# Performance work log

Measured on AMD Instinct MI355X. Metric: run time of the kernel, lower is better.

Reference implementation:

```python
import jax, jax.numpy as jnp
import numpy as np

B, N, C, K, T = 64, 1024, 256, 512, 64
D_THRESH = 0.5
POWER_ITERS = 20


def _pdist(x):
    # x: [..., K, 3] -> pairwise euclidean distances [..., K, K]
    n = jnp.sum(x * x, axis=-1)
    sq = n[..., :, None] + n[..., None, :] - 2.0 * jnp.einsum('...kc,...lc->...kl', x, x)
    return jnp.sqrt(jnp.maximum(sq, 0.0) + 1e-12)


def _forward(rt, rt_centroids, rt_cls_attn, shift_and_scale, W_in, b_in, W1, b1, W2, b2,
             num_rt, anc_idx, pos_idx, neg_idx):
    valid = jnp.arange(N)[None, :] < num_rt[:, None]                      # [B,N]
    # Normalize.batch_unnormalize: pts * scale + shift on valid tokens
    shift = shift_and_scale[:, None, :3]
    scale = shift_and_scale[:, None, 3:4]
    cent = jnp.where(valid[..., None], rt_centroids * scale + shift, rt_centroids)
    attn = jnp.where(valid, rt_cls_attn, -1e9)
    _, top_idx = jax.lax.top_k(attn, K)                                   # [B,K]
    cent_k = jnp.take_along_axis(cent, top_idx[..., None], axis=1)        # [B,K,3]
    rt_k = jnp.take_along_axis(rt, top_idx[..., None], axis=1)            # [B,K,C]
    # SGV padding mask [T,2,K,K]: rows masked by anchor count, cols by pos/neg counts
    n_eff = jnp.minimum(num_rt, K)
    r = jnp.arange(K)
    row_mask = r[None, :] < n_eff[anc_idx][:, None]                       # [T,K]
    col_mask = jnp.stack([r[None, :] < n_eff[pos_idx][:, None],
                          r[None, :] < n_eff[neg_idx][:, None]], axis=1)  # [T,2,K]
    mask = row_mask[:, None, :, None] & col_mask[:, :, None, :]           # [T,2,K,K]
    # input_linear on anchor / neighbour relay tokens
    anc_f = rt_k[anc_idx] @ W_in + b_in                                   # [T,K,C]
    nn_f = jnp.stack([rt_k[pos_idx], rt_k[neg_idx]], axis=1) @ W_in + b_in  # [T,2,K,C]
    anc_c = cent_k[anc_idx]                                               # [T,K,3]
    nn_c = jnp.stack([cent_k[pos_idx], cent_k[neg_idx]], axis=1)          # [T,2,K,3]
    # feature-space nearest-neighbour correspondences anc -> nn (SpectralGV style)
    fd = (jnp.sum(anc_f ** 2, -1)[:, None, :, None]
          + jnp.sum(nn_f ** 2, -1)[:, :, None, :]
          - 2.0 * jnp.einsum('tkc,tnlc->tnkl', anc_f, nn_f))              # [T,2,K,K]
    corr = jnp.argmin(fd, axis=-1)                                        # [T,2,K]
    q_c = jnp.take_along_axis(nn_c, corr[..., None], axis=2)              # [T,2,K,3]
    q_f = jnp.take_along_axis(nn_f, corr[..., None], axis=2)              # [T,2,K,C]
    # correspondence confidence from feature cosine similarity
    cos = jnp.sum(anc_f[:, None] * q_f, -1) / (
        jnp.linalg.norm(anc_f, axis=-1)[:, None] * jnp.linalg.norm(q_f, axis=-1) + 1e-8)
    s = jax.nn.relu(cos)                                                  # [T,2,K]
    # threshold-masked geometric consistency adjacency
    d_p = _pdist(anc_c)[:, None]                                          # [T,1,K,K]
    d_q = _pdist(q_c)                                                     # [T,2,K,K]
    geo = (jnp.abs(d_p - d_q) < D_THRESH) & mask & (~jnp.eye(K, dtype=bool))
    A = geo.astype(jnp.float32) * s[..., :, None] * s[..., None, :]       # [T,2,K,K]
    # leading eigenvector via power iteration (A is entrywise nonnegative)
    v = jnp.full((T, 2, K), 1.0 / np.sqrt(K), dtype=jnp.float32)
    for _ in range(POWER_ITERS):
        w = jnp.einsum('tnkl,tnl->tnk', A, v)
        v = w / (jnp.linalg.norm(w, axis=-1, keepdims=True) + 1e-8)
    eig = -jnp.sort(-v, axis=-1)                                          # sort_eigvec, descending
    h = jax.nn.relu(eig @ W1 + b1)
    scores = jax.nn.sigmoid(h @ W2 + b2)                                  # [T,2,1]
    targets = jnp.zeros_like(scores).at[:, 0].set(1.0)
    return scores, targets


def setup_inputs() -> dict:
    key = jax.random.key(0)
    ks = jax.random.split(key, 12)
    return {
        'rt': jax.random.normal(ks[0], (B, N, C), jnp.float32),
        'rt_centroids': jax.random.normal(ks[1], (B, N, 3), jnp.float32),
        'rt_cls_attn': jax.random.uniform(ks[2], (B, N), jnp.float32),
        'shift_and_scale': jax.random.uniform(ks[3], (B, 4), jnp.float32),
        'num_rt': jax.random.randint(ks[4], (B,), 128, N, jnp.int32),
        'anc_idx': jax.random.randint(ks[5], (T,), 0, B, jnp.int32),
        'pos_idx': jax.random.randint(ks[6], (T,), 0, B, jnp.int32),
        'neg_idx': jax.random.randint(ks[7], (T,), 0, B, jnp.int32),
        'W_in': jax.random.normal(ks[8], (C, C), jnp.float32) / np.sqrt(C),
        'b_in': jnp.zeros((C,), jnp.float32),
        'W1': jax.random.normal(ks[9], (K, K), jnp.float32) / np.sqrt(K),
        'b1': jnp.zeros((K,), jnp.float32),
        'W2': jax.random.normal(ks[10], (K, 1), jnp.float32) / np.sqrt(K),
        'b2': jnp.zeros((1,), jnp.float32),
    }


def reference(rt, rt_centroids, rt_cls_attn, shift_and_scale, num_rt, anc_idx, pos_idx, neg_idx,
              W_in, b_in, W1, b1, W2, b2):
    return _forward(rt, rt_centroids, rt_cls_attn, shift_and_scale, W_in, b_in, W1, b1, W2, b2,
                    num_rt, anc_idx, pos_idx, neg_idx)
```

## Files before the change

### kernel.cpp

```cpp
#include <hip/hip_runtime.h>
#include <cstddef>

#define BB 64
#define NN 1024
#define CC 256
#define KK 512
#define TT 64
#define NPAIR 128

typedef _Float16 h8 __attribute__((ext_vector_type(8)));
typedef _Float16 h4 __attribute__((ext_vector_type(4)));
typedef float f4 __attribute__((ext_vector_type(4)));

typedef __attribute__((address_space(1))) const void GV;
typedef __attribute__((address_space(3))) void LV;
#define GLDS16(g, s) __builtin_amdgcn_global_load_lds((GV*)(const void*)(g), (LV*)(void*)(s), 16, 0, 0)


__global__ __launch_bounds__(256) void wtrans_kernel(
    const float* __restrict__ Win, _Float16* __restrict__ wth, _Float16* __restrict__ wtl)
{
    __shared__ float t[64][65];
    const int k0 = blockIdx.x * 64, n0 = blockIdx.y * 64;
    const int tid = threadIdx.x;
    const int c = tid & 63, r0 = tid >> 6;
    for (int r = r0; r < 64; r += 4)
        t[r][c] = Win[(size_t)(k0 + r) * CC + n0 + c];
    __syncthreads();
    for (int r = r0; r < 64; r += 4) {
        float x = t[c][r];
        _Float16 h = (_Float16)x;
        size_t o = (size_t)(n0 + r) * CC + k0 + c;
        wth[o] = h;
        wtl[o] = (_Float16)(x - (float)h);
    }
}

__global__ __launch_bounds__(512) void sel_kernel(
    const float* __restrict__ attn, const float* __restrict__ cents,
    const float* __restrict__ sas, const int* __restrict__ num_rt,
    int* __restrict__ topidx, int* __restrict__ neff, float* __restrict__ centk)
{
    __shared__ unsigned long long keys[1024];
    const int b = blockIdx.x, tid = threadIdx.x;
    const int nr = num_rt[b];
    for (int i = tid; i < 1024; i += 512) {
        float a = (i < nr) ? attn[b * NN + i] : -1e9f;
        unsigned u = __float_as_uint(a);
        u = (u & 0x80000000u) ? ~u : (u | 0x80000000u);
        keys[i] = ((unsigned long long)u << 32) | (unsigned)(0xFFFFFFFFu - (unsigned)i);
    }
    __syncthreads();
    for (int k = 2; k <= 1024; k <<= 1) {
        for (int j = k >> 1; j > 0; j >>= 1) {
            int i = ((tid & ~(j - 1)) << 1) | (tid & (j - 1));
            int p = i | j;
            unsigned long long a = keys[i], c = keys[p];
            bool up = (i & k) == 0;
            if (up ? (a < c) : (a > c)) { keys[i] = c; keys[p] = a; }
            __syncthreads();
        }
    }
    {
        unsigned long long key = keys[tid];
        int idx = (int)(~(unsigned)key);
        float x = cents[(b * NN + idx) * 3 + 0];
        float y = cents[(b * NN + idx) * 3 + 1];
        float z = cents[(b * NN + idx) * 3 + 2];
        if (idx < nr) {
            float sc = sas[b * 4 + 3];
            x = x * sc + sas[b * 4 + 0];
            y = y * sc + sas[b * 4 + 1];
            z = z * sc + sas[b * 4 + 2];
        }
        float nc = x * x + y * y + z * z;
        ((float4*)centk)[b * KK + tid] = make_float4(x, y, z, nc);
        topidx[b * KK + tid] = idx;
    }
    if (tid == 0) neff[b] = (nr < KK) ? nr : KK;
}

__global__ __launch_bounds__(256) void feat_mfma(
    const float* __restrict__ rt, const int* __restrict__ topidx,
    const _Float16* __restrict__ wth, const _Float16* __restrict__ wtl,
    const float* __restrict__ bin,
    _Float16* __restrict__ feath, _Float16* __restrict__ featl)
{
    const int mtile = blockIdx.x, nt = blockIdx.y;
    __shared__ _Float16 Ah[128][32], Al[128][32], Bh[128][32], Bl[128][32];
    __shared__ int tix[128];
    const int tid = threadIdx.x;
    const int w = tid >> 6, lane = tid & 63;
    const int quad = lane >> 4, l16 = lane & 15;
    const int wm = (w >> 1) * 64, wl = (w & 1) * 64;
    const int b = mtile >> 2;
    if (tid < 128) tix[tid] = topidx[mtile * 128 + tid];
    __syncthreads();
    const int arow_i = tid >> 1;
    const int aseg = (tid & 1) * 16;
    const float* arow = rt + ((size_t)b * NN + tix[arow_i]) * CC + aseg;
    _Float16* bsh = (w < 2) ? &Bh[0][0] : &Bl[0][0];
    const _Float16* bplane = (w < 2) ? wth : wtl;
    const int rowi = lane >> 2, chunk = lane & 3;

    f4 acc[4][4];
    #pragma unroll
    for (int i = 0; i < 4; i++)
        #pragma unroll
        for (int j = 0; j < 4; j++)
            acc[i][j] = (f4){0.f, 0.f, 0.f, 0.f};

    for (int k0 = 0; k0 < CC; k0 += 32) {
        __syncthreads();
        #pragma unroll
        for (int jj = 0; jj < 4; jj++) {
            int j = (w & 1) * 4 + jj;
            int row = j * 16 + rowi;
            GLDS16(bplane + (size_t)(nt * 128 + row) * CC + k0 + chunk * 8, bsh + j * 512);
        }
        {
            const float4* src = (const float4*)(arow + k0);
            #pragma unroll
            for (int c = 0; c < 2; c++) {
                float4 p = src[2 * c], q2 = src[2 * c + 1];
                float xv[8] = {p.x, p.y, p.z, p.w, q2.x, q2.y, q2.z, q2.w};
                h8 hv, lv;
                #pragma unroll
                for (int j = 0; j < 8; j++) {
                    _Float16 h = (_Float16)xv[j];
                    hv[j] = h;
                    lv[j] = (_Float16)(xv[j] - (float)h);
                }
                *(h8*)&Ah[arow_i][aseg + c * 8] = hv;
                *(h8*)&Al[arow_i][aseg + c * 8] = lv;
            }
        }
        __syncthreads();
        h8 afh[4], afl[4], bfh[4], bfl[4];
        #pragma unroll
        for (int i = 0; i < 4; i++) {
            int ra = wm + i * 16 + l16;
            int rb = wl + i * 16 + l16;
            afh[i] = *(const h8*)&Ah[ra][quad * 8];
            afl[i] = *(const h8*)&Al[ra][quad * 8];
            bfh[i] = *(const h8*)&Bh[rb][quad * 8];
            bfl[i] = *(const h8*)&Bl[rb][quad * 8];
        }
        #pragma unroll
        for (int i = 0; i < 4; i++)
            #pragma unroll
            for (int j = 0; j < 4; j++) {
                acc[i][j] = __builtin_amdgcn_mfma_f32_16x16x32_f16(afh[i], bfh[j], acc[i][j], 0, 0, 0);
                acc[i][j] = __builtin_amdgcn_mfma_f32_16x16x32_f16(afh[i], bfl[j], acc[i][j], 0, 0, 0);
                acc[i][j] = __builtin_amdgcn_mfma_f32_16x16x32_f16(afl[i], bfh[j], acc[i][j], 0, 0, 0);
            }
    }
    #pragma unroll
    for (int j = 0; j < 4; j++) {
        int col = wl + j * 16 + l16;
        float bj = bin[nt * 128 + col];
        #pragma unroll
        for (int i = 0; i < 4; i++)
            #pragma unroll
            for (int r = 0; r < 4; r++) {
                int row = wm + i * 16 + quad * 4 + r;
                float v = acc[i][j][r] + bj;
                _Float16 h = (_Float16)v;
                size_t o = (size_t)(mtile * 128 + row) * CC + nt * 128 + col;
                feath[o] = h;
                featl[o] = (_Float16)(v - (float)h);
            }
    }
}

__global__ __launch_bounds__(256) void norm_kernel(
    const _Float16* __restrict__ feath, const _Float16* __restrict__ featl,
    float* __restrict__ normF)
{
    int r = blockIdx.x * 4 + (threadIdx.x >> 6);
    int lane = threadIdx.x & 63;
    h4 hv = ((const h4*)(feath + (size_t)r * CC))[lane];
    h4 lv = ((const h4*)(featl + (size_t)r * CC))[lane];
    float s = 0.f;
    #pragma unroll
    for (int j = 0; j < 4; j++) {
        float x = (float)hv[j] + (float)lv[j];
        s += x * x;
    }
    for (int off = 32; off; off >>= 1) s += __shfl_down(s, off);
    if (lane == 0) normF[r] = s;
}

__global__ __launch_bounds__(256) void argmin_mfma(
    const _Float16* __restrict__ feath, const _Float16* __restrict__ featl,
    const float* __restrict__ normF,
    const int* __restrict__ anc, const int* __restrict__ pos, const int* __restrict__ neg,
    float* __restrict__ partv, int* __restrict__ partl, float* __restrict__ partd)
{
    const int lt = blockIdx.x, kt = blockIdx.y, pr = blockIdx.z;
    const int t = pr >> 1, nn2 = pr & 1;
    const int a = anc[t];
    const int bb = nn2 ? neg[t] : pos[t];
    const size_t Abase = ((size_t)a * KK + kt * 128) * CC;
    const size_t Bbase = ((size_t)bb * KK + lt * 128) * CC;
    __shared__ _Float16 Ah[128][32], Al[128][32], Bh[128][32], Bl[128][32];
    __shared__ float rdv[128][2];
    __shared__ int   rdl[128][2];
    __shared__ float rdd[128][2];
    const int tid = threadIdx.x;
    const int w = tid >> 6, lane = tid & 63;
    const int quad = lane >> 4, l16 = lane & 15;
    const int wm = (w >> 1) * 64, wl = (w & 1) * 64;
    const int rowi = lane >> 2, chunk = lane & 3;
    const _Float16* gplane = (w == 0) ? feath + Abase : (w == 1) ? featl + Abase
                           : (w == 2) ? feath + Bbase : featl + Bbase;
    _Float16* splane = (w == 0) ? &Ah[0][0] : (w == 1) ? &Al[0][0]
                     : (w == 2) ? &Bh[0][0] : &Bl[0][0];
    const _Float16* grow = gplane + (size_t)rowi * CC + chunk * 8;

    f4 acc[4][4];
    #pragma unroll
    for (int i = 0; i < 4; i++)
        #pragma unroll
        for (int j = 0; j < 4; j++)
            acc[i][j] = (f4){0.f, 0.f, 0.f, 0.f};

    for (int k0 = 0; k0 < CC; k0 += 32) {
        __syncthreads();
        #pragma unroll
        for (int j = 0; j < 8; j++)
            GLDS16(grow + (size_t)(j * 16) * CC + k0, splane + j * 512);
        __syncthreads();
        h8 afh[4], afl[4], bfh[4], bfl[4];
        #pragma unroll
        for (int i = 0; i < 4; i++) {
            int ra = wm + i * 16 + l16;
            int rb = wl + i * 16 + l16;
            afh[i] = *(const h8*)&Ah[ra][quad * 8];
            afl[i] = *(const h8*)&Al[ra][quad * 8];
            bfh[i] = *(const h8*)&Bh[rb][quad * 8];
            bfl[i] = *(const h8*)&Bl[rb][quad * 8];
        }
        #pragma unroll
        for (int i = 0; i < 4; i++)
            #pragma unroll
            for (int j = 0; j < 4; j++) {
                acc[i][j] = __builtin_amdgcn_mfma_f32_16x16x32_f16(afh[i], bfh[j], acc[i][j], 0, 0, 0);
                acc[i][j] = __builtin_amdgcn_mfma_f32_16x16x32_f16(afh[i], bfl[j], acc[i][j], 0, 0, 0);
                acc[i][j] = __builtin_amdgcn_mfma_f32_16x16x32_f16(afl[i], bfh[j], acc[i][j], 0, 0, 0);
            }
    }
    float nbj[4];
    #pragma unroll
    for (int j = 0; j < 4; j++)
        nbj[j] = normF[(size_t)bb * KK + lt * 128 + wl + j * 16 + l16];
    #pragma unroll
    for (int i = 0; i < 4; i++) {
        #pragma unroll
        for (int r = 0; r < 4; r++) {
            float bv = INFINITY; int bl = 0; float bd = 0.f;
            #pragma unroll
            for (int j = 0; j < 4; j++) {
                float d = acc[i][j][r];
                float v = nbj[j] - 2.f * d;
                int l = lt * 128 + wl + j * 16 + l16;
                if (v < bv) { bv = v; bl = l; bd = d; }
            }
            #pragma unroll
            for (int off = 1; off < 16; off <<= 1) {
                float ov = __shfl_xor(bv, off);
                int   ol = __shfl_xor(bl, off);
                float od = __shfl_xor(bd, off);
                if (ov < bv || (ov == bv && ol < bl)) { bv = ov; bl = ol; bd = od; }
            }
            if (l16 == 0) {
                int row = wm + i * 16 + quad * 4 + r;
                rdv[row][w & 1] = bv;
                rdl[row][w & 1] = bl;
                rdd[row][w & 1] = bd;
            }
        }
    }
    __syncthreads();
    if (tid < 128) {
        float bv = rdv[tid][0]; int bl = rdl[tid][0]; float bd = rdd[tid][0];
        float v1 = rdv[tid][1]; int l1 = rdl[tid][1];
        if (v1 < bv || (v1 == bv && l1 < bl)) { bv = v1; bl = l1; bd = rdd[tid][1]; }
        size_t idx = (((size_t)pr * 4 + kt) * 128 + tid) * 4 + lt;
        partv[idx] = bv; partl[idx] = bl; partd[idx] = bd;
    }
}

__global__ __launch_bounds__(256) void geo_kernel(
    const float* __restrict__ centk,
    const float* __restrict__ partv, const int* __restrict__ partl,
    const float* __restrict__ partd, const float* __restrict__ normF,
    const int* __restrict__ neff,
    const int* __restrict__ anc, const int* __restrict__ pos, const int* __restrict__ neg,
    float* __restrict__ sbuf, unsigned* __restrict__ gmask)
{
    const int kt = blockIdx.x;
    const int lt4 = blockIdx.y;
    const int pair = blockIdx.z;
    const int t = pair >> 1, nn2 = pair & 1;
    const int a = anc[t];
    const int bb2 = (nn2 == 0) ? pos[t] : neg[t];
    const int nea = neff[a], neb = neff[bb2];
    const bool writer = (kt == 0) && (lt4 == 0);
    __shared__ int ci[512];
    __shared__ __align__(16) float4 ca[512], cq[512];
    for (int i = threadIdx.x; i < KK; i += 256) {
        size_t base = ((size_t)pair * KK + i) * 4;
        float bv = partv[base]; int bl = partl[base]; float bd = partd[base];
        #pragma unroll
        for (int lt = 1; lt < 4; lt++) {
            float v = partv[base + lt]; int l = partl[base + lt];
            if (v < bv || (v == bv && l < bl)) { bv = v; bl = l; bd = partd[base + lt]; }
        }
        ci[i] = bl;
        if (writer) {
            float na = normF[(size_t)a * KK + i];
            float nb = normF[(size_t)bb2 * KK + bl];
            float cosv = bd / (sqrtf(na) * sqrtf(nb) + 1e-8f);
            sbuf[pair * KK + i] = fmaxf(cosv, 0.f);
        }
    }
    __syncthreads();
    for (int i = threadIdx.x; i < KK; i += 256) {
        ca[i] = ((const float4*)centk)[a * KK + i];
        cq[i] = ((const float4*)centk)[bb2 * KK + ci[i]];
    }
    __syncthreads();
    const int k = kt * 256 + threadIdx.x;
    float4 pk = ca[k], qk = cq[k];
    bool rowm = k < nea;
    unsigned* outp = gmask + ((size_t)pair * KK + k) * 16 + lt4 * 4;
    for (int w = 0; w < 4; w++) {
        unsigned word = 0;
        #pragma unroll
        for (int bi = 0; bi < 32; bi++) {
            int l = lt4 * 128 + w * 32 + bi;
            float4 pl = ca[l], ql = cq[l];
            float dp2 = pk.w + pl.w - 2.f * (pk.x * pl.x + pk.y * pl.y + pk.z * pl.z);
            float dp = sqrtf(fmaxf(dp2, 0.f) + 1e-12f);
            float dq2 = qk.w + ql.w - 2.f * (qk.x * ql.x + qk.y * ql.y + qk.z * ql.z);
            float dq = sqrtf(fmaxf(dq2, 0.f) + 1e-12f);
            bool g = (fabsf(dp - dq) < 0.5f) && rowm && (l < neb) && (l != k);
            word |= (g ? (1u << bi) : 0u);
        }
        outp[w] = word;
    }
}

__global__ __launch_bounds__(1024, 4) void power_kernel(
    const unsigned* __restrict__ gmask, const float* __restrict__ sbuf,
    const float* __restrict__ W1, const float* __restrict__ b1,
    const float* __restrict__ W2, const float* __restrict__ b2,
    float* __restrict__ out)
{
    const int pair = blockIdx.x;
    const int tid = threadIdx.x;
    const int row = tid & 511;
    const int half = tid >> 9;
    __shared__ __align__(16) float u[512];
    __shared__ float T[64][257];
    __shared__ float pacc[1024];
    __shared__ float red[16];
    __shared__ float ev[512];
    __shared__ float hpart[1024];
    unsigned m[8];
    const unsigned* g = gmask + ((size_t)pair * KK + row) * 16 + half * 8;
    #pragma unroll
    for (int w = 0; w < 8; w++) m[w] = g[w];
    const float s = sbuf[pair * KK + row];
    const int bp = tid & 63;
    const int vh = tid >> 6;
    const int GV_[16] = {0,1,3,2,6,7,5,4,12,13,15,14,10,11,9,8};
    const int GB[15] = {0,1,0,2,0,1,0,3,0,1,0,2,0,1,0};
    const float GS[15] = {1.f,1.f,-1.f,1.f,1.f,-1.f,-1.f,1.f,1.f,1.f,-1.f,-1.f,1.f,-1.f,-1.f};
    float v = 0.044194173824159216f;
    if (half == 0) u[row] = s * v;
    __syncthreads();
    for (int it = 0; it < 20; it++) {
        {
            float4 ulo = *(const float4*)&u[bp * 8];
            float4 uhi = *(const float4*)&u[bp * 8 + 4];
            float ul[4] = {ulo.x, ulo.y, ulo.z, ulo.w};
            float H = 0.f;
            H += (float)((vh >> 0) & 1) * uhi.x;
            H += (float)((vh >> 1) & 1) * uhi.y;
            H += (float)((vh >> 2) & 1) * uhi.z;
            H += (float)((vh >> 3) & 1) * uhi.w;
            float L = 0.f;
            T[bp][vh * 16 + 0] = H;
            #pragma unroll
            for (int k = 1; k < 16; k++) {
                L += GS[k - 1] * ul[GB[k - 1]];
                T[bp][vh * 16 + GV_[k]] = H + L;
            }
        }
        __syncthreads();
        float a0 = 0.f, a1 = 0.f, a2 = 0.f, a3 = 0.f;
        #pragma unroll
        for (int w = 0; w < 8; w++) {
            unsigned mw = m[w];
            const int p0 = half * 32 + w * 4;
            a0 += T[p0 + 0][mw & 255u];
            a1 += T[p0 + 1][(mw >> 8) & 255u];
            a2 += T[p0 + 2][(mw >> 16) & 255u];
            a3 += T[p0 + 3][mw >> 24];
        }
        pacc[tid] = (a0 + a1) + (a2 + a3);
        __syncthreads();
        float wk = s * (pacc[row] + pacc[row + 512]);
        float t2 = wk * wk;
        for (int off = 32; off; off >>= 1) t2 += __shfl_down(t2, off);
        if ((tid & 63) == 0) red[tid >> 6] = t2;
        __syncthreads();
        float tot = 0.f;
        #pragma unroll
        for (int x = 0; x < 16; x++) tot += red[x];
        tot *= 0.5f;
        v = wk / (sqrtf(tot) + 1e-8f);
        if (half == 0) u[row] = s * v;
        __syncthreads();
    }
    if (half == 0) ev[row] = v;
    __syncthreads();
    for (int kk = 2; kk <= 512; kk <<= 1) {
        for (int j = kk >> 1; j; j >>= 1) {
            if (tid < 256) {
                int i = ((tid & ~(j - 1)) << 1) | (tid & (j - 1));
                int p = i | j;
                float x = ev[i], y = ev[p];
                bool up = (i & kk) == 0;
                if (up ? (x < y) : (x > y)) { ev[i] = y; ev[p] = x; }
            }
            __syncthreads();
        }
    }
    const int cbase = half * 256;
    float h = (half == 0) ? b1[row] : 0.f;
    #pragma unroll 8
    for (int l = 0; l < 256; l++)
        h += ev[cbase + l] * W1[(size_t)(cbase + l) * KK + row];
    hpart[tid] = h;
    __syncthreads();
    float term = 0.f;
    if (half == 0) {
        float hv = fmaxf(hpart[row] + hpart[row + 512], 0.f);
        term = hv * W2[row];
    }
    for (int off = 32; off; off >>= 1) term += __shfl_down(term, off);
    if ((tid & 63) == 0) red[tid >> 6] = term;
    __syncthreads();
    if (tid == 0) {
        float sc = 0.f;
        #pragma unroll
        for (int x = 0; x < 16; x++) sc += red[x];
        sc += b2[0];
        out[pair] = 1.f / (1.f + expf(-sc));
        out[NPAIR + pair] = (pair & 1) ? 0.f : 1.f;
    }
}

extern "C" void kernel_launch(void* const* d_in, const int* in_sizes, int n_in,
                              void* d_out, int out_size, void* d_ws, size_t ws_size,
                              hipStream_t stream) {
    (void)in_sizes; (void)n_in; (void)out_size; (void)ws_size;
    const float* rt    = (const float*)d_in[0];
    const float* cents = (const float*)d_in[1];
    const float* attn  = (const float*)d_in[2];
    const float* sas   = (const float*)d_in[3];
    const int* num_rt  = (const int*)d_in[4];
    const int* anc     = (const int*)d_in[5];
    const int* pos     = (const int*)d_in[6];
    const int* neg     = (const int*)d_in[7];
    const float* Win   = (const float*)d_in[8];
    const float* bin   = (const float*)d_in[9];
    const float* W1    = (const float*)d_in[10];
    const float* b1    = (const float*)d_in[11];
    const float* W2    = (const float*)d_in[12];
    const float* b2    = (const float*)d_in[13];

    float* ws = (float*)d_ws;
    _Float16* feath = (_Float16*)ws;
    _Float16* featl = (_Float16*)(ws + 4194304);
    float* normF = ws + 8388608;
    float* centk = ws + 8421376;
    float* sbuf  = ws + 8552448;
    int* topidx  = (int*)(ws + 8617984);
    int* neffp   = (int*)(ws + 8650752);
    unsigned* gmask = (unsigned*)(ws + 8716352);
    _Float16* wth = (_Float16*)(ws + 8716352 + 786432);
    _Float16* wtl = (_Float16*)(ws + 8716352 + 819200);
    float* partv = (float*)(ws + 9764928);
    int*   partl = (int*)(ws + 10027072);
    float* partd = (float*)(ws + 10289216);
    float* out = (float*)d_out;

    wtrans_kernel<<<dim3(4, 4), 256, 0, stream>>>(Win, wth, wtl);
    sel_kernel<<<64, 512, 0, stream>>>(attn, cents, sas, num_rt, topidx, neffp, centk);
    feat_mfma<<<dim3(256, 2), 256, 0, stream>>>(rt, topidx, wth, wtl, bin, feath, featl);
    norm_kernel<<<8192, 256, 0, stream>>>(feath, featl, normF);
    argmin_mfma<<<dim3(4, 4, 128), 256, 0, stream>>>(feath, featl, normF, anc, pos, neg, partv, partl, partd);
    geo_kernel<<<dim3(2, 4, 128), 256, 0, stream>>>(centk, partv, partl, partd, normF, neffp, anc, pos, neg, sbuf, gmask);
    power_kernel<<<128, 1024, 0, stream>>>(gmask, sbuf, W1, b1, W2, b2, out);
}
```

Measured before the change: 378.1 us.

## Double-buffer LDS tiles in argmin MFMA kernel to overlap loads with compute

Replaces the single-buffered shared-memory tiles in the feature-distance argmin kernel with a two-stage ping-pong buffer. The next K-slice is fetched with global_load_lds while MFMAs run on the current slice, and one barrier per iteration replaces two. The reduction scratch arrays now alias the first tile buffer. Shared memory per block doubles to 64KB, which may lower occupancy.

```diff
diff --git a/kernel.cpp b/kernel.cpp
--- a/kernel.cpp
+++ b/kernel.cpp
@@ -203,10 +203,10 @@
     const int bb = nn2 ? neg[t] : pos[t];
     const size_t Abase = ((size_t)a * KK + kt * 128) * CC;
     const size_t Bbase = ((size_t)bb * KK + lt * 128) * CC;
-    __shared__ _Float16 Ah[128][32], Al[128][32], Bh[128][32], Bl[128][32];
-    __shared__ float rdv[128][2];
-    __shared__ int   rdl[128][2];
-    __shared__ float rdd[128][2];
+    __shared__ _Float16 S[2][4][4096];
+    float* rdv = (float*)&S[0][0][0];
+    int*   rdl = (int*)(rdv + 256);
+    float* rdd = (float*)(rdl + 256);
     const int tid = threadIdx.x;
     const int w = tid >> 6, lane = tid & 63;
     const int quad = lane >> 4, l16 = lane & 15;
@@ -214,8 +214,6 @@
     const int rowi = lane >> 2, chunk = lane & 3;
     const _Float16* gplane = (w == 0) ? feath + Abase : (w == 1) ? featl + Abase
                            : (w == 2) ? feath + Bbase : featl + Bbase;
-    _Float16* splane = (w == 0) ? &Ah[0][0] : (w == 1) ? &Al[0][0]
-                     : (w == 2) ? &Bh[0][0] : &Bl[0][0];
     const _Float16* grow = gplane + (size_t)rowi * CC + chunk * 8;
 
     f4 acc[4][4];
@@ -225,21 +223,32 @@
         for (int j = 0; j < 4; j++)
             acc[i][j] = (f4){0.f, 0.f, 0.f, 0.f};
 
+    #pragma unroll
+    for (int j = 0; j < 8; j++)
+        GLDS16(grow + (size_t)(j * 16) * CC, &S[0][w][j * 512]);
+    __syncthreads();
+
+    int cur = 0;
     for (int k0 = 0; k0 < CC; k0 += 32) {
-        __syncthreads();
-        #pragma unroll
-        for (int j = 0; j < 8; j++)
-            GLDS16(grow + (size_t)(j * 16) * CC + k0, splane + j * 512);
-        __syncthreads();
+        const int k1 = k0 + 32;
+        if (k1 < CC) {
+            #pragma unroll
+            for (int j = 0; j < 8; j++)
+                GLDS16(grow + (size_t)(j * 16) * CC + k1, &S[cur ^ 1][w][j * 512]);
+        }
+        const _Float16* Ahc = &S[cur][0][0];
+        const _Float16* Alc = &S[cur][1][0];
+        const _Float16* Bhc = &S[cur][2][0];
+        const _Float16* Blc = &S[cur][3][0];
         h8 afh[4], afl[4], bfh[4], bfl[4];
         #pragma unroll
         for (int i = 0; i < 4; i++) {
             int ra = wm + i * 16 + l16;
             int rb = wl + i * 16 + l16;
-            afh[i] = *(const h8*)&Ah[ra][quad * 8];
-            afl[i] = *(const h8*)&Al[ra][quad * 8];
-            bfh[i] = *(const h8*)&Bh[rb][quad * 8];
-            bfl[i] = *(const h8*)&Bl[rb][quad * 8];
+            afh[i] = *(const h8*)&Ahc[ra * 32 + quad * 8];
+            afl[i] = *(const h8*)&Alc[ra * 32 + quad * 8];
+            bfh[i] = *(const h8*)&Bhc[rb * 32 + quad * 8];
+            bfl[i] = *(const h8*)&Blc[rb * 32 + quad * 8];
         }
         #pragma unroll
         for (int i = 0; i < 4; i++)
@@ -249,6 +258,8 @@
                 acc[i][j] = __builtin_amdgcn_mfma_f32_16x16x32_f16(afh[i], bfl[j], acc[i][j], 0, 0, 0);
                 acc[i][j] = __builtin_amdgcn_mfma_f32_16x16x32_f16(afl[i], bfh[j], acc[i][j], 0, 0, 0);
             }
+        __syncthreads();
+        cur ^= 1;
     }
     float nbj[4];
     #pragma unroll
@@ -275,17 +286,17 @@
             }
             if (l16 == 0) {
                 int row = wm + i * 16 + quad * 4 + r;
-                rdv[row][w & 1] = bv;
-                rdl[row][w & 1] = bl;
-                rdd[row][w & 1] = bd;
+                rdv[row * 2 + (w & 1)] = bv;
+                rdl[row * 2 + (w & 1)] = bl;
+                rdd[row * 2 + (w & 1)] = bd;
             }
         }
     }
     __syncthreads();
     if (tid < 128) {
-        float bv = rdv[tid][0]; int bl = rdl[tid][0]; float bd = rdd[tid][0];
-        float v1 = rdv[tid][1]; int l1 = rdl[tid][1];
-        if (v1 < bv || (v1 == bv && l1 < bl)) { bv = v1; bl = l1; bd = rdd[tid][1]; }
+        float bv = rdv[tid * 2 + 0]; int bl = rdl[tid * 2 + 0]; float bd = rdd[tid * 2 + 0];
+        float v1 = rdv[tid * 2 + 1]; int l1 = rdl[tid * 2 + 1];
+        if (v1 < bv || (v1 == bv && l1 < bl)) { bv = v1; bl = l1; bd = rdd[tid * 2 + 1]; }
         size_t idx = (((size_t)pr * 4 + kt) * 128 + tid) * 4 + lt;
         partv[idx] = bv; partl[idx] = bl; partd[idx] = bd;
     }
```

Result: faster. 366.4 us (-3.1%).

## Enlarge argmin MFMA tiles to 256x256 with double-buffered LDS and XCD-aware block mapping

Applied to the files above, without the earlier changes.

The argmin GEMM kernel now uses 512-thread blocks that each compute a 256x256 tile instead of 128x128. LDS loads are double-buffered so the next k-slice streams in while MFMAs run, with explicit vmcnt waits and raw barriers. Block ids are remapped so each pair's tiles land on the same XCD for L2 reuse. The partial-result layout shrinks from 4 to 2 column tiles, and geo_kernel is updated to match. The cost is higher register pressure (acc[4][8]) and 64KB+ of LDS, which lowers occupancy.

```diff
diff --git a/kernel.cpp b/kernel.cpp
--- a/kernel.cpp
+++ b/kernel.cpp
@@ -191,79 +191,99 @@
     if (lane == 0) normF[r] = s;
 }
 
-__global__ __launch_bounds__(256) void argmin_mfma(
+__global__ __launch_bounds__(512) void argmin_mfma(
     const _Float16* __restrict__ feath, const _Float16* __restrict__ featl,
     const float* __restrict__ normF,
     const int* __restrict__ anc, const int* __restrict__ pos, const int* __restrict__ neg,
     float* __restrict__ partv, int* __restrict__ partl, float* __restrict__ partd)
 {
-    const int lt = blockIdx.x, kt = blockIdx.y, pr = blockIdx.z;
+    const int id = blockIdx.x;
+    const int xcd = id & 7, kgrp = id >> 3;
+    const int pr = xcd * 16 + (kgrp >> 2);
+    const int s = kgrp & 3;
+    const int lt = s & 1, kt = s >> 1;
     const int t = pr >> 1, nn2 = pr & 1;
     const int a = anc[t];
     const int bb = nn2 ? neg[t] : pos[t];
-    const size_t Abase = ((size_t)a * KK + kt * 128) * CC;
-    const size_t Bbase = ((size_t)bb * KK + lt * 128) * CC;
-    __shared__ _Float16 Ah[128][32], Al[128][32], Bh[128][32], Bl[128][32];
-    __shared__ float rdv[128][2];
-    __shared__ int   rdl[128][2];
-    __shared__ float rdd[128][2];
+    const size_t Abase = ((size_t)a * KK + kt * 256) * CC;
+    const size_t Bbase = ((size_t)bb * KK + lt * 256) * CC;
+    __shared__ _Float16 S[2][4][8192];
+    __shared__ float rdv[256][2];
+    __shared__ int   rdl[256][2];
+    __shared__ float rdd[256][2];
     const int tid = threadIdx.x;
     const int w = tid >> 6, lane = tid & 63;
     const int quad = lane >> 4, l16 = lane & 15;
-    const int wm = (w >> 1) * 64, wl = (w & 1) * 64;
+    const int wr = w >> 1, wc = w & 1;
     const int rowi = lane >> 2, chunk = lane & 3;
-    const _Float16* gplane = (w == 0) ? feath + Abase : (w == 1) ? featl + Abase
-                           : (w == 2) ? feath + Bbase : featl + Bbase;
-    _Float16* splane = (w == 0) ? &Ah[0][0] : (w == 1) ? &Al[0][0]
-                     : (w == 2) ? &Bh[0][0] : &Bl[0][0];
-    const _Float16* grow = gplane + (size_t)rowi * CC + chunk * 8;
-
-    f4 acc[4][4];
+    const int plane = w >> 1;
+    const int srow = (w & 1) * 128;
+    const _Float16* gsrc = (plane == 0) ? feath + Abase
+                         : (plane == 1) ? featl + Abase
+                         : (plane == 2) ? feath + Bbase
+                         :                featl + Bbase;
+    const _Float16* grow = gsrc + (size_t)(srow + rowi) * CC + chunk * 8;
+
+    f4 acc[4][8];
     #pragma unroll
     for (int i = 0; i < 4; i++)
         #pragma unroll
-        for (int j = 0; j < 4; j++)
+        for (int j = 0; j < 8; j++)
             acc[i][j] = (f4){0.f, 0.f, 0.f, 0.f};
 
-    for (int k0 = 0; k0 < CC; k0 += 32) {
-        __syncthreads();
-        #pragma unroll
-        for (int j = 0; j < 8; j++)
-            GLDS16(grow + (size_t)(j * 16) * CC + k0, splane + j * 512);
-        __syncthreads();
-        h8 afh[4], afl[4], bfh[4], bfl[4];
+    #pragma unroll
+    for (int j = 0; j < 8; j++)
+        GLDS16(grow + (size_t)(j * 16) * CC, &S[0][plane][srow * 32 + j * 512]);
+
+    #pragma unroll
+    for (int kk = 0; kk < 8; kk++) {
+        const int cb = kk & 1;
+        if (kk < 7) {
+            const int k1 = (kk + 1) * 32;
+            #pragma unroll
+            for (int j = 0; j < 8; j++)
+                GLDS16(grow + (size_t)(j * 16) * CC + k1, &S[cb ^ 1][plane][srow * 32 + j * 512]);
+            asm volatile("s_waitcnt vmcnt(8)" ::: "memory");
+        } else {
+            asm volatile("s_waitcnt vmcnt(0)" ::: "memory");
+        }
+        __builtin_amdgcn_s_barrier();
+        h8 afh[4], afl[4];
         #pragma unroll
         for (int i = 0; i < 4; i++) {
-            int ra = wm + i * 16 + l16;
-            int rb = wl + i * 16 + l16;
-            afh[i] = *(const h8*)&Ah[ra][quad * 8];
-            afl[i] = *(const h8*)&Al[ra][quad * 8];
-            bfh[i] = *(const h8*)&Bh[rb][quad * 8];
-            bfl[i] = *(const h8*)&Bl[rb][quad * 8];
-        }
-        #pragma unroll
-        for (int i = 0; i < 4; i++)
-            #pragma unroll
-            for (int j = 0; j < 4; j++) {
-                acc[i][j] = __builtin_amdgcn_mfma_f32_16x16x32_f16(afh[i], bfh[j], acc[i][j], 0, 0, 0);
-                acc[i][j] = __builtin_amdgcn_mfma_f32_16x16x32_f16(afh[i], bfl[j], acc[i][j], 0, 0, 0);
-                acc[i][j] = __builtin_amdgcn_mfma_f32_16x16x32_f16(afl[i], bfh[j], acc[i][j], 0, 0, 0);
-            }
-    }
-    float nbj[4];
-    #pragma unroll
-    for (int j = 0; j < 4; j++)
-        nbj[j] = normF[(size_t)bb * KK + lt * 128 + wl + j * 16 + l16];
+            int ra = wr * 64 + i * 16 + l16;
+            afh[i] = *(const h8*)&S[cb][0][ra * 32 + quad * 8];
+            afl[i] = *(const h8*)&S[cb][1][ra * 32 + quad * 8];
+        }
+        #pragma unroll
+        for (int j = 0; j < 8; j++) {
+            int rb = wc * 128 + j * 16 + l16;
+            h8 bfh = *(const h8*)&S[cb][2][rb * 32 + quad * 8];
+            h8 bfl = *(const h8*)&S[cb][3][rb * 32 + quad * 8];
+            #pragma unroll
+            for (int i = 0; i < 4; i++) {
+                acc[i][j] = __builtin_amdgcn_mfma_f32_16x16x32_f16(afh[i], bfh, acc[i][j], 0, 0, 0);
+                acc[i][j] = __builtin_amdgcn_mfma_f32_16x16x32_f16(afh[i], bfl, acc[i][j], 0, 0, 0);
+                acc[i][j] = __builtin_amdgcn_mfma_f32_16x16x32_f16(afl[i], bfh, acc[i][j], 0, 0, 0);
+            }
+        }
+        __builtin_amdgcn_sched_barrier(0);
+        __builtin_amdgcn_s_barrier();
+    }
+    float nbj[8];
+    #pragma unroll
+    for (int j = 0; j < 8; j++)
+        nbj[j] = normF[(size_t)bb * KK + lt * 256 + wc * 128 + j * 16 + l16];
     #pragma unroll
     for (int i = 0; i < 4; i++) {
         #pragma unroll
         for (int r = 0; r < 4; r++) {
             float bv = INFINITY; int bl = 0; float bd = 0.f;
             #pragma unroll
-            for (int j = 0; j < 4; j++) {
+            for (int j = 0; j < 8; j++) {
                 float d = acc[i][j][r];
                 float v = nbj[j] - 2.f * d;
-                int l = lt * 128 + wl + j * 16 + l16;
+                int l = lt * 256 + wc * 128 + j * 16 + l16;
                 if (v < bv) { bv = v; bl = l; bd = d; }
             }
             #pragma unroll
@@ -274,19 +294,19 @@
                 if (ov < bv || (ov == bv && ol < bl)) { bv = ov; bl = ol; bd = od; }
             }
             if (l16 == 0) {
-                int row = wm + i * 16 + quad * 4 + r;
-                rdv[row][w & 1] = bv;
-                rdl[row][w & 1] = bl;
-                rdd[row][w & 1] = bd;
-            }
-        }
-    }
-    __syncthreads();
-    if (tid < 128) {
+                int row = wr * 64 + i * 16 + quad * 4 + r;
+                rdv[row][wc] = bv;
+                rdl[row][wc] = bl;
+                rdd[row][wc] = bd;
+            }
+        }
+    }
+    __syncthreads();
+    if (tid < 256) {
         float bv = rdv[tid][0]; int bl = rdl[tid][0]; float bd = rdd[tid][0];
         float v1 = rdv[tid][1]; int l1 = rdl[tid][1];
         if (v1 < bv || (v1 == bv && l1 < bl)) { bv = v1; bl = l1; bd = rdd[tid][1]; }
-        size_t idx = (((size_t)pr * 4 + kt) * 128 + tid) * 4 + lt;
+        size_t idx = ((size_t)pr * KK + kt * 256 + tid) * 2 + lt;
         partv[idx] = bv; partl[idx] = bl; partd[idx] = bd;
     }
 }
@@ -310,13 +330,10 @@
     __shared__ int ci[512];
     __shared__ __align__(16) float4 ca[512], cq[512];
     for (int i = threadIdx.x; i < KK; i += 256) {
-        size_t base = ((size_t)pair * KK + i) * 4;
+        size_t base = ((size_t)pair * KK + i) * 2;
         float bv = partv[base]; int bl = partl[base]; float bd = partd[base];
-        #pragma unroll
-        for (int lt = 1; lt < 4; lt++) {
-            float v = partv[base + lt]; int l = partl[base + lt];
-            if (v < bv || (v == bv && l < bl)) { bv = v; bl = l; bd = partd[base + lt]; }
-        }
+        float v = partv[base + 1]; int l = partl[base + 1];
+        if (v < bv || (v == bv && l < bl)) { bv = v; bl = l; bd = partd[base + 1]; }
         ci[i] = bl;
         if (writer) {
             float na = normF[(size_t)a * KK + i];
@@ -503,7 +520,7 @@
     sel_kernel<<<64, 512, 0, stream>>>(attn, cents, sas, num_rt, topidx, neffp, centk);
     feat_mfma<<<dim3(256, 2), 256, 0, stream>>>(rt, topidx, wth, wtl, bin, feath, featl);
     norm_kernel<<<8192, 256, 0, stream>>>(feath, featl, normF);
-    argmin_mfma<<<dim3(4, 4, 128), 256, 0, stream>>>(feath, featl, normF, anc, pos, neg, partv, partl, partd);
+    argmin_mfma<<<512, 512, 0, stream>>>(feath, featl, normF, anc, pos, neg, partv, partl, partd);
     geo_kernel<<<dim3(2, 4, 128), 256, 0, stream>>>(centk, partv, partl, partd, normF, neffp, anc, pos, neg, sbuf, gmask);
     power_kernel<<<128, 1024, 0, stream>>>(gmask, sbuf, W1, b1, W2, b2, out);
 }
```

After: 349.8 us. 1.08x faster.
